# Kernel tuning notes

Hardware: AMD Instinct MI355X
Metric: run time of the kernel (lower is better)

Reference implementation:

```python
import jax, jax.numpy as jnp
import numpy as np

B, S, DMAX, NMEL, DM, K = 8, 100, 12, 80, 128, 9
T = S * DMAX  # 1200 max mel frames
EPS = 1e-5  # BatchNorm eps (eval mode, running_mean=0, running_var=1)


def setup_inputs() -> dict:
    key = jax.random.key(0)
    ks = jax.random.split(key, 16)
    durations = jax.random.randint(ks[0], (B, S), 4, DMAX + 1).astype(jnp.int32)
    mel_len = jnp.sum(durations, axis=1).astype(jnp.int32)
    src_len = jnp.full((B,), S, dtype=jnp.int32)
    mel = jax.random.normal(ks[1], (B, T, NMEL), dtype=jnp.float32)
    # conv stack params (xavier-ish uniform)
    s1 = float(np.sqrt(6.0 / (1 * K + DM * K)))
    w1 = jax.random.uniform(ks[2], (DM, 1, 1, K), minval=-s1, maxval=s1, dtype=jnp.float32)
    g1 = 1.0 + 0.1 * jax.random.normal(ks[3], (DM,), dtype=jnp.float32)
    be1 = 0.1 * jax.random.normal(ks[4], (DM,), dtype=jnp.float32)
    s2 = float(np.sqrt(6.0 / (DM * K + 1 * K)))
    w2 = jax.random.uniform(ks[5], (1, DM, 1, K), minval=-s2, maxval=s2, dtype=jnp.float32)
    g2 = 1.0 + 0.1 * jax.random.normal(ks[6], (1,), dtype=jnp.float32)
    be2 = 0.1 * jax.random.normal(ks[7], (1,), dtype=jnp.float32)
    # BiGRU params (pytorch layout: gates [r|z|n] stacked -> 3*H rows)
    sh = float(1.0 / np.sqrt(DM))
    u = lambda k, shape: jax.random.uniform(k, shape, minval=-sh, maxval=sh, dtype=jnp.float32)
    w_ih_f = u(ks[8], (3 * DM, NMEL)); w_hh_f = u(ks[9], (3 * DM, DM))
    b_ih_f = u(ks[10], (3 * DM,));    b_hh_f = u(ks[11], (3 * DM,))
    w_ih_b = u(ks[12], (3 * DM, NMEL)); w_hh_b = u(ks[13], (3 * DM, DM))
    b_ih_b = u(ks[14], (3 * DM,));    b_hh_b = u(ks[15], (3 * DM,))
    return {"mel": mel, "durations": durations, "mel_len": mel_len, "src_len": src_len,
            "w1": w1, "g1": g1, "be1": be1, "w2": w2, "g2": g2, "be2": be2,
            "w_ih_f": w_ih_f, "w_hh_f": w_hh_f, "b_ih_f": b_ih_f, "b_hh_f": b_hh_f,
            "w_ih_b": w_ih_b, "w_hh_b": w_hh_b, "b_ih_b": b_ih_b, "b_hh_b": b_hh_b}


def _bn_eval(x, g, b):
    # eval-mode BatchNorm2d with running_mean=0, running_var=1; x [B,C,T,M]
    scale = g / jnp.sqrt(1.0 + EPS)
    return x * scale[None, :, None, None] + b[None, :, None, None]


def _gru_scan(xs_seq, reset_seq, w_hh, b_hh):
    # xs_seq [T,B,3H] precomputed input projections; reset_seq [T,B] 1.0 -> reset h to 0
    H = w_hh.shape[1]
    Bn = xs_seq.shape[1]

    def step(h, inp):
        xg, rst = inp
        h = h * (1.0 - rst)[:, None]
        hg = h @ w_hh.T + b_hh
        xr, xz, xn = jnp.split(xg, 3, axis=-1)
        hr, hz, hn = jnp.split(hg, 3, axis=-1)
        r = jax.nn.sigmoid(xr + hr)
        z = jax.nn.sigmoid(xz + hz)
        n = jnp.tanh(xn + r * hn)
        h_new = (1.0 - z) * n + z * h
        return h_new, h_new

    h0 = jnp.zeros((Bn, H), xs_seq.dtype)
    _, hs = jax.lax.scan(step, h0, (xs_seq, reset_seq))
    return hs  # [T,B,H]


def reference(mel, durations, mel_len, src_len, w1, g1, be1, w2, g2, be2,
              w_ih_f, w_hh_f, b_ih_f, b_hh_f, w_ih_b, w_hh_b, b_ih_b, b_hh_b):
    pad = (K - 1) // 2
    # conv stack: kernel (1,K) mixes only the mel-channel axis -> apply to full mel once
    x = mel[:, None, :, :]  # [B,1,T,M]
    x = jax.lax.conv_general_dilated(x, w1, (1, 1), [(0, 0), (pad, pad)])
    x = jax.nn.relu(_bn_eval(x, g1, be1))
    x = jax.lax.conv_general_dilated(x, w2, (1, 1), [(0, 0), (pad, pad)])
    x = jax.nn.relu(_bn_eval(x, g2, be2))
    x = x[:, 0]  # [B,T,M]

    # segment boundaries from durations (all phones valid here, durations > 0)
    cum = jnp.cumsum(durations, axis=1)      # [B,S]
    starts = cum - durations                 # segment start frame per phone
    ends = cum - 1                           # segment end frame per phone
    bidx = jnp.arange(B)[:, None]
    start_mask = jnp.zeros((B, T), x.dtype).at[bidx, starts].set(1.0)
    end_mask = jnp.zeros((B, T), x.dtype).at[bidx, ends].set(1.0)

    # forward direction: reset h at segment starts, read h at segment ends
    xf = jnp.einsum('btm,gm->tbg', x, w_ih_f) + b_ih_f
    Hf = _gru_scan(xf, start_mask.T, w_hh_f, b_hh_f)           # [T,B,H]
    # backward direction: scan reversed time, reset at original segment ends
    xb = jnp.einsum('btm,gm->tbg', x, w_ih_b) + b_ih_b
    Hb = _gru_scan(xb[::-1], end_mask.T[::-1], w_hh_b, b_hh_b)[::-1]  # [T,B,H], orig time

    hf = jnp.take_along_axis(jnp.transpose(Hf, (1, 0, 2)), ends[..., None], axis=1)    # [B,S,H]
    hb = jnp.take_along_axis(jnp.transpose(Hb, (1, 0, 2)), starts[..., None], axis=1)  # [B,S,H]
    out = jnp.concatenate([hf, hb], axis=-1)  # [B,S,2H]
    valid = (jnp.arange(S)[None, :] < src_len[:, None])[..., None]
    return jnp.where(valid, out, 0.0)
```

## Files before the change

kernel.cpp:

```cpp
#include <hip/hip_runtime.h>
#include <math.h>

#define BB   8
#define SS   100
#define TT   1200
#define NM   80
#define DMC  128
#define KK   9
#define G3   384
#define NROW (BB*TT)

typedef __attribute__((ext_vector_type(8))) short short8;
typedef __attribute__((ext_vector_type(4))) float f32x4;

__device__ __forceinline__ float sigmoid_(float v) { return 1.f / (1.f + __expf(-v)); }
__device__ __forceinline__ float tanh_(float v) {
    float a = fabsf(v);
    float e = __expf(-2.f * a);
    float t = (1.f - e) / (1.f + e);
    return copysignf(t, v);
}
__device__ __forceinline__ unsigned short f2bf(float f) {
    unsigned int u = __float_as_uint(f);
    unsigned int r = (u + 0x7fffu + ((u >> 16) & 1u)) >> 16;
    return (unsigned short)r;
}

__global__ __launch_bounds__(1024) void k_prep(
    const float* __restrict__ whf, const float* __restrict__ whb,
    const float* __restrict__ wif, const float* __restrict__ wib,
    const float* __restrict__ bf, const float* __restrict__ bbv,
    const int* __restrict__ dur,
    unsigned short* __restrict__ wph, unsigned short* __restrict__ wpl,
    unsigned short* __restrict__ wih_h, unsigned short* __restrict__ wih_l,
    float* __restrict__ biasc, int* __restrict__ starts) {
    int blk = blockIdx.x;
    int tid = threadIdx.x;
    if (blk < 12) {
        int idx = blk * 1024 + tid;
        int lane = idx & 63;
        int k32  = (idx >> 6) & 3;
        int tau  = (idx >> 8) % 24;
        int dir  = idx / (24 * 4 * 64);
        const float* w = dir ? whb : whf;
        int g = tau * 16 + (lane & 15);
        int kbase = k32 * 32 + (lane >> 4) * 8;
#pragma unroll
        for (int j = 0; j < 8; j++) {
            float v = w[g * DMC + kbase + j];
            unsigned short hi = f2bf(v);
            float hif = __uint_as_float(((unsigned)hi) << 16);
            unsigned short lo = f2bf(v - hif);
            wph[idx * 8 + j] = hi;
            wpl[idx * 8 + j] = lo;
        }
    } else if (blk < 21) {
        int idx = (blk - 12) * 1024 + tid;
        int lane = idx & 63;
        int ks   = (idx >> 6) % 3;
        int tau  = idx / (3 * 64);
        int gate = tau * 16 + (lane & 15);
        int kb   = ks * 32 + (lane >> 4) * 8;
        const float* w = (gate < G3) ? (wif + gate * NM) : (wib + (gate - G3) * NM);
#pragma unroll
        for (int j = 0; j < 8; j++) {
            int k = kb + j;
            float v = (k < NM) ? w[k] : 0.f;
            unsigned short hi = f2bf(v);
            float hif = __uint_as_float(((unsigned)hi) << 16);
            unsigned short lo = f2bf(v - hif);
            wih_h[idx * 8 + j] = hi;
            wih_l[idx * 8 + j] = lo;
        }
    } else {
        __shared__ int buf[BB][128];
        int s = tid & 127, b = tid >> 7;
        int v = (s < SS) ? dur[b * SS + s] : 0;
        buf[b][s] = v;
        __syncthreads();
        for (int off = 1; off < 128; off <<= 1) {
            int t = (s >= off) ? buf[b][s - off] : 0;
            __syncthreads();
            buf[b][s] += t;
            __syncthreads();
        }
        if (s < SS) starts[b * SS + s] = buf[b][s] - v;
        if (tid < 768) biasc[tid] = (tid < G3) ? bf[tid] : bbv[tid - G3];
    }
}

__global__ __launch_bounds__(256) void k_conv(
    const float* __restrict__ mel, const int* __restrict__ mel_len,
    const float* __restrict__ w1, const float* __restrict__ g1, const float* __restrict__ be1,
    const float* __restrict__ w2, const float* __restrict__ g2, const float* __restrict__ be2,
    float* __restrict__ xout) {
    int b = blockIdx.y;
    int t = blockIdx.x;
    int ml = mel_len[b];
    if (t >= ml) return;

    __shared__ __align__(16) float mp[96];
    __shared__ __align__(16) float part[8][84];

    int tid = threadIdx.x;
    int mq = tid >> 6, g = tid & 63;
    int ms = 20 * mq;
    const float inv_sqrt = 0.9999950000374997f;

    if (tid < 96) {
        float v = 0.f;
        if (tid >= 8 && tid < 88) v = mel[(b * TT + t) * NM + tid - 8];
        mp[tid] = v;
    }
    __syncthreads();

    float c[20];
#pragma unroll
    for (int m = 0; m < 20; m++) c[m] = 0.f;

#pragma unroll 1
    for (int dd = 0; dd < 2; dd++) {
        int d = g + 64 * dd;
        float sc = g1[d] * inv_sqrt;
        float w1r[KK], w2r[KK];
#pragma unroll
        for (int k = 0; k < KK; k++) { w1r[k] = w1[d * KK + k] * sc; w2r[k] = w2[d * KK + k]; }
        float sb = be1[d];

        float mw[12];
        {
            const float4* p4 = (const float4*)(mp + ms);
            float4 a = p4[0], bq = p4[1], cq = p4[2];
            mw[0]=a.x;  mw[1]=a.y;  mw[2]=a.z;  mw[3]=a.w;
            mw[4]=bq.x; mw[5]=bq.y; mw[6]=bq.z; mw[7]=bq.w;
            mw[8]=cq.x; mw[9]=cq.y; mw[10]=cq.z; mw[11]=cq.w;
        }
#pragma unroll
        for (int ch = 0; ch < 7; ch++) {
#pragma unroll
            for (int jj = 0; jj < 4; jj++) {
                int off = ch * 4 + jj;
                float yv = sb;
#pragma unroll
                for (int k = 0; k < KK; k++) yv = fmaf(w1r[k], mw[jj + k], yv);
                yv = fmaxf(yv, 0.f);
                int j = ms + off;
                if (j < 4 || j >= 84) yv = 0.f;
#pragma unroll
                for (int k = 0; k < KK; k++) {
                    int mo = off - k;
                    if (mo >= 0 && mo < 20) c[mo] = fmaf(w2r[k], yv, c[mo]);
                }
            }
            if (ch < 6) {
#pragma unroll
                for (int q = 0; q < 8; q++) mw[q] = mw[q + 4];
                const float4* p4 = (const float4*)(mp + ms + ch * 4 + 12);
                float4 a = p4[0];
                mw[8]=a.x; mw[9]=a.y; mw[10]=a.z; mw[11]=a.w;
            }
        }
    }

#pragma unroll
    for (int m = 0; m < 20; m++) {
        c[m] += __shfl_xor(c[m], 1);
        c[m] += __shfl_xor(c[m], 2);
        c[m] += __shfl_xor(c[m], 4);
    }
    if ((g & 7) == 0) {
        int p = g >> 3;
#pragma unroll
        for (int m = 0; m < 20; m += 4)
            *(float4*)&part[p][ms + m] = make_float4(c[m], c[m+1], c[m+2], c[m+3]);
    }
    __syncthreads();

    if (tid < 80) {
        float s = 0.f;
#pragma unroll
        for (int p = 0; p < 8; p++) s += part[p][tid];
        float v = fmaxf(0.f, fmaf(s, g2[0] * inv_sqrt, be2[0]));
        xout[(b * TT + t) * NM + tid] = v;
    }
}

__global__ __launch_bounds__(256) void k_proj(
    const float* __restrict__ x,
    const unsigned short* __restrict__ wih_h, const unsigned short* __restrict__ wih_l,
    const float* __restrict__ biasc,
    float* __restrict__ xall) {
    __shared__ short8 bhs[2 * 3 * 64];
    __shared__ short8 bls[2 * 3 * 64];

    int tid = threadIdx.x;
    int wave = tid >> 6, lane = tid & 63, quad = lane >> 4;
    int row0 = blockIdx.x * 32;
    int tau0 = blockIdx.y * 24;

    for (int i = tid; i < 2 * 3 * 64; i += 256) {
        int rg = i / 192, rem = i - rg * 192;
        int ks = rem >> 6, ln = rem & 63;
        int row = row0 + rg * 16 + (ln & 15);
        int kb = ks * 32 + (ln >> 4) * 8;
        short8 hi8, lo8;
#pragma unroll
        for (int j = 0; j < 8; j++) {
            int k = kb + j;
            float v = (k < NM) ? x[row * NM + k] : 0.f;
            unsigned short hi = f2bf(v);
            float hif = __uint_as_float(((unsigned)hi) << 16);
            hi8[j] = (short)hi;
            lo8[j] = (short)f2bf(v - hif);
        }
        bhs[i] = hi8;
        bls[i] = lo8;
    }
    __syncthreads();

    const short8* wih_h8 = (const short8*)wih_h;
    const short8* wih_l8 = (const short8*)wih_l;

    for (int tt = 0; tt < 6; tt++) {
        int tau = tau0 + wave * 6 + tt;
        short8 Ah[3], Al[3];
#pragma unroll
        for (int ks = 0; ks < 3; ks++) {
            int ia = (tau * 3 + ks) * 64 + lane;
            Ah[ks] = wih_h8[ia];
            Al[ks] = wih_l8[ia];
        }
        f32x4 acc0 = (f32x4){0.f,0.f,0.f,0.f}, acc1 = (f32x4){0.f,0.f,0.f,0.f};
#pragma unroll
        for (int ks = 0; ks < 3; ks++) {
            short8 Bh0 = bhs[ks * 64 + lane],       Bl0 = bls[ks * 64 + lane];
            short8 Bh1 = bhs[192 + ks * 64 + lane], Bl1 = bls[192 + ks * 64 + lane];
            acc0 = __builtin_amdgcn_mfma_f32_16x16x32_bf16(Ah[ks], Bh0, acc0, 0, 0, 0);
            acc0 = __builtin_amdgcn_mfma_f32_16x16x32_bf16(Ah[ks], Bl0, acc0, 0, 0, 0);
            acc0 = __builtin_amdgcn_mfma_f32_16x16x32_bf16(Al[ks], Bh0, acc0, 0, 0, 0);
            acc1 = __builtin_amdgcn_mfma_f32_16x16x32_bf16(Ah[ks], Bh1, acc1, 0, 0, 0);
            acc1 = __builtin_amdgcn_mfma_f32_16x16x32_bf16(Ah[ks], Bl1, acc1, 0, 0, 0);
            acc1 = __builtin_amdgcn_mfma_f32_16x16x32_bf16(Al[ks], Bh1, acc1, 0, 0, 0);
        }
        float4 bias4 = *(const float4*)&biasc[tau * 16 + quad * 4];
        int ga = tau * 16 + quad * 4;
        int rowA = row0 + (lane & 15);
        float4 o0 = make_float4(acc0[0] + bias4.x, acc0[1] + bias4.y,
                                acc0[2] + bias4.z, acc0[3] + bias4.w);
        *(float4*)&xall[rowA * 768 + ga] = o0;
        int rowB = rowA + 16;
        float4 o1 = make_float4(acc1[0] + bias4.x, acc1[1] + bias4.y,
                                acc1[2] + bias4.z, acc1[3] + bias4.w);
        *(float4*)&xall[rowB * 768 + ga] = o1;
    }
}

__global__ __launch_bounds__(512) void k_gru(
    const float* __restrict__ xall,
    const unsigned short* __restrict__ wph, const unsigned short* __restrict__ wpl,
    const int* __restrict__ dur_all, const int* __restrict__ starts,
    const int* __restrict__ src_len,
    const float* __restrict__ bhf, const float* __restrict__ bhb,
    float* __restrict__ out) {
    int sblk = blockIdx.x;
    int b    = blockIdx.y;
    int dir  = blockIdx.z;
    int s0 = sblk * 16;

    __shared__ __align__(16) unsigned short hbh[2][2048];
    __shared__ __align__(16) unsigned short hbl[2][2048];

    int tid  = threadIdx.x;
    int wave = tid >> 6, lane = tid & 63;
    int quad = lane >> 4, seg = lane & 15;

    for (int i = tid; i < 2048; i += 512) {
        hbh[0][i] = 0; hbl[0][i] = 0; hbh[1][i] = 0; hbl[1][i] = 0;
    }

    short8 Ah[3][4], Al[3][4];
    const short8* wph8 = (const short8*)wph;
    const short8* wpl8 = (const short8*)wpl;
#pragma unroll
    for (int tt = 0; tt < 3; tt++)
#pragma unroll
        for (int k32 = 0; k32 < 4; k32++) {
            int tau = wave + 8 * tt;
            int idx = ((dir * 24 + tau) * 4 + k32) * 64 + lane;
            Ah[tt][k32] = wph8[idx];
            Al[tt][k32] = wpl8[idx];
        }

    int s = s0 + seg;
    int sd = (s < SS) ? dur_all[b * SS + s] : 0;
    int st = (s < SS) ? starts[b * SS + s]  : 0;
    int slb = src_len[b];
    const float* bh = dir ? bhb : bhf;
    int j0 = wave * 16 + quad * 4;
    float4 bhr = *(const float4*)&bh[j0];
    float4 bhz = *(const float4*)&bh[DMC + j0];
    float4 bhn = *(const float4*)&bh[2 * DMC + j0];
    float4 h = make_float4(0.f, 0.f, 0.f, 0.f);

    int idx8 = (j0 >> 5) * 64 + ((j0 >> 3) & 3) * 16 + seg;
    int wbase = idx8 * 8 + (j0 & 7);

    __syncthreads();

    for (int i = 0; i < 12; i++) {
        int p = i & 1;
        bool act = (i < sd);

        float4 xr = make_float4(0.f,0.f,0.f,0.f), xz = xr, xn = xr;
        if (act) {
            int t = dir ? (st + sd - 1 - i) : (st + i);
            const float* xrow = xall + (size_t)(b * TT + t) * 768 + dir * G3 + j0;
            xr = *(const float4*)&xrow[0];
            xz = *(const float4*)&xrow[DMC];
            xn = *(const float4*)&xrow[2 * DMC];
        }

        f32x4 acc[3];
#pragma unroll
        for (int tt = 0; tt < 3; tt++) acc[tt] = (f32x4){0.f, 0.f, 0.f, 0.f};
#pragma unroll
        for (int k32 = 0; k32 < 4; k32++) {
            short8 Bh = ((const short8*)hbh[p])[k32 * 64 + lane];
            short8 Bl = ((const short8*)hbl[p])[k32 * 64 + lane];
#pragma unroll
            for (int tt = 0; tt < 3; tt++) {
                acc[tt] = __builtin_amdgcn_mfma_f32_16x16x32_bf16(Ah[tt][k32], Bh, acc[tt], 0, 0, 0);
                acc[tt] = __builtin_amdgcn_mfma_f32_16x16x32_bf16(Ah[tt][k32], Bl, acc[tt], 0, 0, 0);
                acc[tt] = __builtin_amdgcn_mfma_f32_16x16x32_bf16(Al[tt][k32], Bh, acc[tt], 0, 0, 0);
            }
        }

        if (act) {
            float hv[4] = {h.x, h.y, h.z, h.w};
            float xrv[4] = {xr.x, xr.y, xr.z, xr.w};
            float xzv[4] = {xz.x, xz.y, xz.z, xz.w};
            float xnv[4] = {xn.x, xn.y, xn.z, xn.w};
            float bhrv[4] = {bhr.x, bhr.y, bhr.z, bhr.w};
            float bhzv[4] = {bhz.x, bhz.y, bhz.z, bhz.w};
            float bhnv[4] = {bhn.x, bhn.y, bhn.z, bhn.w};
#pragma unroll
            for (int cmp = 0; cmp < 4; cmp++) {
                float r = sigmoid_(xrv[cmp] + acc[0][cmp] + bhrv[cmp]);
                float z = sigmoid_(xzv[cmp] + acc[1][cmp] + bhzv[cmp]);
                float n = tanh_(xnv[cmp] + r * (acc[2][cmp] + bhnv[cmp]));
                hv[cmp] = (1.f - z) * n + z * hv[cmp];
            }
            h = make_float4(hv[0], hv[1], hv[2], hv[3]);
            if (i == sd - 1) {
                float4 vout = (s < slb) ? h : make_float4(0.f, 0.f, 0.f, 0.f);
                *(float4*)&out[(b * SS + s) * (2 * DMC) + dir * DMC + j0] = vout;
            }
        }

        {
            float hv[4] = {h.x, h.y, h.z, h.w};
            ushort4 hi4, lo4;
            unsigned short hs_[4], ls_[4];
#pragma unroll
            for (int cmp = 0; cmp < 4; cmp++) {
                unsigned short hi = f2bf(hv[cmp]);
                float hif = __uint_as_float(((unsigned)hi) << 16);
                hs_[cmp] = hi;
                ls_[cmp] = f2bf(hv[cmp] - hif);
            }
            hi4 = make_ushort4(hs_[0], hs_[1], hs_[2], hs_[3]);
            lo4 = make_ushort4(ls_[0], ls_[1], ls_[2], ls_[3]);
            *(ushort4*)&hbh[1 - p][wbase] = hi4;
            *(ushort4*)&hbl[1 - p][wbase] = lo4;
        }
        __syncthreads();
    }
}

extern "C" void kernel_launch(void* const* d_in, const int* in_sizes, int n_in,
                              void* d_out, int out_size, void* d_ws, size_t ws_size,
                              hipStream_t stream) {
    const float* mel      = (const float*)d_in[0];
    const int*   durations= (const int*)  d_in[1];
    const int*   mel_len  = (const int*)  d_in[2];
    const int*   src_len  = (const int*)  d_in[3];
    const float* w1       = (const float*)d_in[4];
    const float* g1       = (const float*)d_in[5];
    const float* be1      = (const float*)d_in[6];
    const float* w2       = (const float*)d_in[7];
    const float* g2       = (const float*)d_in[8];
    const float* be2      = (const float*)d_in[9];
    const float* w_ih_f   = (const float*)d_in[10];
    const float* w_hh_f   = (const float*)d_in[11];
    const float* b_ih_f   = (const float*)d_in[12];
    const float* b_hh_f   = (const float*)d_in[13];
    const float* w_ih_b   = (const float*)d_in[14];
    const float* w_hh_b   = (const float*)d_in[15];
    const float* b_ih_b   = (const float*)d_in[16];
    const float* b_hh_b   = (const float*)d_in[17];
    float* out = (float*)d_out;

    float* x    = (float*)d_ws;
    float* xall = x + NROW * NM;
    unsigned short* wph   = (unsigned short*)(xall + NROW * 768);
    unsigned short* wpl   = wph + 2 * 24 * 4 * 64 * 8;
    unsigned short* wih_h = wpl + 2 * 24 * 4 * 64 * 8;
    unsigned short* wih_l = wih_h + 48 * 3 * 64 * 8;
    float* biasc = (float*)(wih_l + 48 * 3 * 64 * 8);
    int*   starts= (int*)(biasc + 768);

    k_prep<<<22, 1024, 0, stream>>>(w_hh_f, w_hh_b, w_ih_f, w_ih_b, b_ih_f, b_ih_b,
                                    durations, wph, wpl, wih_h, wih_l, biasc, starts);
    k_conv<<<dim3(TT, BB), 256, 0, stream>>>(mel, mel_len, w1, g1, be1, w2, g2, be2, x);
    k_proj<<<dim3(NROW / 32, 2), 256, 0, stream>>>(x, wih_h, wih_l, biasc, xall);
    k_gru<<<dim3(7, 8, 2), 512, 0, stream>>>(xall, wph, wpl, durations, starts, src_len,
                                             b_hh_f, b_hh_b, out);
}
```

Before: 181.8 us.

## Rewrite conv stack on MFMA with split-bf16 weights and activations

The two-layer conv stack moves from scalar FMA loops to bf16 MFMA instructions. Each fp32 value is split into a hi and a lo bf16 part and three MFMAs are issued per tile to keep near-fp32 accuracy. k_prep gains two blocks that pre-pack the BN-scaled conv1 weights and the transposed conv2 weights into the MFMA operand layout. Intermediate activations are staged in shared memory, and conv2 is computed as per-tap partial sums that are then summed along diagonals. This adds shared-memory traffic and extra precision-split work per frame.

```diff
diff --git a/kernel.cpp b/kernel.cpp
--- a/kernel.cpp
+++ b/kernel.cpp
@@ -31,9 +31,13 @@
     const float* __restrict__ wif, const float* __restrict__ wib,
     const float* __restrict__ bf, const float* __restrict__ bbv,
     const int* __restrict__ dur,
+    const float* __restrict__ w1, const float* __restrict__ g1,
+    const float* __restrict__ w2,
     unsigned short* __restrict__ wph, unsigned short* __restrict__ wpl,
     unsigned short* __restrict__ wih_h, unsigned short* __restrict__ wih_l,
-    float* __restrict__ biasc, int* __restrict__ starts) {
+    float* __restrict__ biasc, int* __restrict__ starts,
+    unsigned short* __restrict__ w1fh, unsigned short* __restrict__ w1fl,
+    unsigned short* __restrict__ w2th, unsigned short* __restrict__ w2tl) {
     int blk = blockIdx.x;
     int tid = threadIdx.x;
     if (blk < 12) {
@@ -72,7 +76,7 @@
             wih_h[idx * 8 + j] = hi;
             wih_l[idx * 8 + j] = lo;
         }
-    } else {
+    } else if (blk == 21) {
         __shared__ int buf[BB][128];
         int s = tid & 127, b = tid >> 7;
         int v = (s < SS) ? dur[b * SS + s] : 0;
@@ -86,102 +90,149 @@
         }
         if (s < SS) starts[b * SS + s] = buf[b][s] - v;
         if (tid < 768) biasc[tid] = (tid < G3) ? bf[tid] : bbv[tid - G3];
+    } else if (blk == 22) {
+        if (tid < 512) {
+            int dt = tid >> 6, lane = tid & 63;
+            int d = dt * 16 + (lane & 15);
+            float sc = g1[d] * 0.9999950000374997f;
+#pragma unroll
+            for (int j = 0; j < 8; j++) {
+                int k = (lane >> 4) * 8 + j;
+                float v = (k < KK) ? w1[d * KK + k] * sc : 0.f;
+                unsigned short hi = f2bf(v);
+                float hif = __uint_as_float(((unsigned)hi) << 16);
+                w1fh[tid * 8 + j] = hi;
+                w1fl[tid * 8 + j] = f2bf(v - hif);
+            }
+        }
+    } else {
+        if (tid < 256) {
+            int k32 = tid >> 6, lane = tid & 63;
+            int kp = lane & 15;
+#pragma unroll
+            for (int j = 0; j < 8; j++) {
+                int d = k32 * 32 + (lane >> 4) * 8 + j;
+                float v = (kp < KK) ? w2[d * KK + kp] : 0.f;
+                unsigned short hi = f2bf(v);
+                float hif = __uint_as_float(((unsigned)hi) << 16);
+                w2th[tid * 8 + j] = hi;
+                w2tl[tid * 8 + j] = f2bf(v - hif);
+            }
+        }
     }
 }
 
 __global__ __launch_bounds__(256) void k_conv(
     const float* __restrict__ mel, const int* __restrict__ mel_len,
-    const float* __restrict__ w1, const float* __restrict__ g1, const float* __restrict__ be1,
-    const float* __restrict__ w2, const float* __restrict__ g2, const float* __restrict__ be2,
+    const unsigned short* __restrict__ w1fh, const unsigned short* __restrict__ w1fl,
+    const float* __restrict__ be1,
+    const unsigned short* __restrict__ w2th, const unsigned short* __restrict__ w2tl,
+    const float* __restrict__ g2, const float* __restrict__ be2,
     float* __restrict__ xout) {
-    int b = blockIdx.y;
-    int t = blockIdx.x;
-    int ml = mel_len[b];
-    if (t >= ml) return;
-
-    __shared__ __align__(16) float mp[96];
-    __shared__ __align__(16) float part[8][84];
-
-    int tid = threadIdx.x;
-    int mq = tid >> 6, g = tid & 63;
-    int ms = 20 * mq;
-    const float inv_sqrt = 0.9999950000374997f;
+    int b = blockIdx.y, t = blockIdx.x;
+    if (t >= mel_len[b]) return;
+
+    __shared__ __align__(16) unsigned short mh[96], mlo[96];
+    __shared__ __align__(16) unsigned short y1h[96][136], y1l[96][136];
+    __shared__ __align__(16) float gl[96][13];
+
+    int tid = threadIdx.x, wave = tid >> 6, lane = tid & 63;
+    int quad = lane >> 4, col = lane & 15;
+    const float invs = 0.9999950000374997f;
 
     if (tid < 96) {
-        float v = 0.f;
-        if (tid >= 8 && tid < 88) v = mel[(b * TT + t) * NM + tid - 8];
-        mp[tid] = v;
+        float v = (tid >= 4 && tid < 84) ? mel[(b * TT + t) * NM + tid - 4] : 0.f;
+        unsigned short hi = f2bf(v);
+        mh[tid]  = hi;
+        mlo[tid] = f2bf(v - __uint_as_float(((unsigned)hi) << 16));
+    }
+    for (int i = tid; i < 16 * 136; i += 256) {
+        int r = i / 136, c2 = i - r * 136;
+        int row = (r < 4) ? r : 80 + r;
+        y1h[row][c2] = 0; y1l[row][c2] = 0;
     }
     __syncthreads();
 
-    float c[20];
-#pragma unroll
-    for (int m = 0; m < 20; m++) c[m] = 0.f;
-
-#pragma unroll 1
+    const short8* w1fh8 = (const short8*)w1fh;
+    const short8* w1fl8 = (const short8*)w1fl;
+    short8 a1h[2], a1l[2];
+    float4 bb[2];
+#pragma unroll
     for (int dd = 0; dd < 2; dd++) {
-        int d = g + 64 * dd;
-        float sc = g1[d] * inv_sqrt;
-        float w1r[KK], w2r[KK];
-#pragma unroll
-        for (int k = 0; k < KK; k++) { w1r[k] = w1[d * KK + k] * sc; w2r[k] = w2[d * KK + k]; }
-        float sb = be1[d];
-
-        float mw[12];
-        {
-            const float4* p4 = (const float4*)(mp + ms);
-            float4 a = p4[0], bq = p4[1], cq = p4[2];
-            mw[0]=a.x;  mw[1]=a.y;  mw[2]=a.z;  mw[3]=a.w;
-            mw[4]=bq.x; mw[5]=bq.y; mw[6]=bq.z; mw[7]=bq.w;
-            mw[8]=cq.x; mw[9]=cq.y; mw[10]=cq.z; mw[11]=cq.w;
-        }
-#pragma unroll
-        for (int ch = 0; ch < 7; ch++) {
-#pragma unroll
-            for (int jj = 0; jj < 4; jj++) {
-                int off = ch * 4 + jj;
-                float yv = sb;
-#pragma unroll
-                for (int k = 0; k < KK; k++) yv = fmaf(w1r[k], mw[jj + k], yv);
-                yv = fmaxf(yv, 0.f);
-                int j = ms + off;
-                if (j < 4 || j >= 84) yv = 0.f;
-#pragma unroll
-                for (int k = 0; k < KK; k++) {
-                    int mo = off - k;
-                    if (mo >= 0 && mo < 20) c[mo] = fmaf(w2r[k], yv, c[mo]);
-                }
-            }
-            if (ch < 6) {
-#pragma unroll
-                for (int q = 0; q < 8; q++) mw[q] = mw[q + 4];
-                const float4* p4 = (const float4*)(mp + ms + ch * 4 + 12);
-                float4 a = p4[0];
-                mw[8]=a.x; mw[9]=a.y; mw[10]=a.z; mw[11]=a.w;
-            }
-        }
-    }
-
-#pragma unroll
-    for (int m = 0; m < 20; m++) {
-        c[m] += __shfl_xor(c[m], 1);
-        c[m] += __shfl_xor(c[m], 2);
-        c[m] += __shfl_xor(c[m], 4);
-    }
-    if ((g & 7) == 0) {
-        int p = g >> 3;
-#pragma unroll
-        for (int m = 0; m < 20; m += 4)
-            *(float4*)&part[p][ms + m] = make_float4(c[m], c[m+1], c[m+2], c[m+3]);
+        int dt = 2 * wave + dd;
+        a1h[dd] = w1fh8[dt * 64 + lane];
+        a1l[dd] = w1fl8[dt * 64 + lane];
+        bb[dd]  = *(const float4*)&be1[dt * 16 + quad * 4];
+    }
+#pragma unroll
+    for (int nt = 0; nt < 5; nt++) {
+        int mbase = nt * 16 + col;
+        short8 Bh = {0,0,0,0,0,0,0,0}, Bl = {0,0,0,0,0,0,0,0};
+        if (quad == 0) {
+#pragma unroll
+            for (int j = 0; j < 8; j++) {
+                Bh[j] = (short)mh[mbase + j];
+                Bl[j] = (short)mlo[mbase + j];
+            }
+        } else if (quad == 1) {
+            Bh[0] = (short)mh[mbase + 8];
+            Bl[0] = (short)mlo[mbase + 8];
+        }
+#pragma unroll
+        for (int dd = 0; dd < 2; dd++) {
+            f32x4 acc = (f32x4){0.f, 0.f, 0.f, 0.f};
+            acc = __builtin_amdgcn_mfma_f32_16x16x32_bf16(a1h[dd], Bh, acc, 0, 0, 0);
+            acc = __builtin_amdgcn_mfma_f32_16x16x32_bf16(a1h[dd], Bl, acc, 0, 0, 0);
+            acc = __builtin_amdgcn_mfma_f32_16x16x32_bf16(a1l[dd], Bh, acc, 0, 0, 0);
+            int i = mbase + 4;
+            int dbase = (2 * wave + dd) * 16 + quad * 4;
+            float bbv[4] = {bb[dd].x, bb[dd].y, bb[dd].z, bb[dd].w};
+            unsigned short hs4[4], ls4[4];
+#pragma unroll
+            for (int reg = 0; reg < 4; reg++) {
+                float y = fmaxf(acc[reg] + bbv[reg], 0.f);
+                unsigned short hi = f2bf(y);
+                hs4[reg] = hi;
+                ls4[reg] = f2bf(y - __uint_as_float(((unsigned)hi) << 16));
+            }
+            *(ushort4*)&y1h[i][dbase] = make_ushort4(hs4[0], hs4[1], hs4[2], hs4[3]);
+            *(ushort4*)&y1l[i][dbase] = make_ushort4(ls4[0], ls4[1], ls4[2], ls4[3]);
+        }
     }
     __syncthreads();
 
-    if (tid < 80) {
+    const short8* w2th8 = (const short8*)w2th;
+    const short8* w2tl8 = (const short8*)w2tl;
+    short8 a2h[4], a2l[4];
+#pragma unroll
+    for (int k32 = 0; k32 < 4; k32++) {
+        a2h[k32] = w2th8[k32 * 64 + lane];
+        a2l[k32] = w2tl8[k32 * 64 + lane];
+    }
+    for (int nn = wave; nn < 6; nn += 4) {
+        int i = nn * 16 + col;
+        f32x4 acc = (f32x4){0.f, 0.f, 0.f, 0.f};
+#pragma unroll
+        for (int k32 = 0; k32 < 4; k32++) {
+            short8 Bh = *(const short8*)&y1h[i][k32 * 32 + quad * 8];
+            short8 Bl = *(const short8*)&y1l[i][k32 * 32 + quad * 8];
+            acc = __builtin_amdgcn_mfma_f32_16x16x32_bf16(a2h[k32], Bh, acc, 0, 0, 0);
+            acc = __builtin_amdgcn_mfma_f32_16x16x32_bf16(a2h[k32], Bl, acc, 0, 0, 0);
+            acc = __builtin_amdgcn_mfma_f32_16x16x32_bf16(a2l[k32], Bh, acc, 0, 0, 0);
+        }
+#pragma unroll
+        for (int reg = 0; reg < 4; reg++) {
+            int kp = quad * 4 + reg;
+            if (kp < KK) gl[i][kp] = acc[reg];
+        }
+    }
+    __syncthreads();
+
+    if (tid < NM) {
         float s = 0.f;
 #pragma unroll
-        for (int p = 0; p < 8; p++) s += part[p][tid];
-        float v = fmaxf(0.f, fmaf(s, g2[0] * inv_sqrt, be2[0]));
-        xout[(b * TT + t) * NM + tid] = v;
+        for (int k = 0; k < KK; k++) s += gl[tid + k][k];
+        xout[(b * TT + t) * NM + tid] = fmaxf(0.f, fmaf(s, g2[0] * invs, be2[0]));
     }
 }
 
@@ -359,7 +410,6 @@
 
         {
             float hv[4] = {h.x, h.y, h.z, h.w};
-            ushort4 hi4, lo4;
             unsigned short hs_[4], ls_[4];
 #pragma unroll
             for (int cmp = 0; cmp < 4; cmp++) {
@@ -368,10 +418,8 @@
                 hs_[cmp] = hi;
                 ls_[cmp] = f2bf(hv[cmp] - hif);
             }
-            hi4 = make_ushort4(hs_[0], hs_[1], hs_[2], hs_[3]);
-            lo4 = make_ushort4(ls_[0], ls_[1], ls_[2], ls_[3]);
-            *(ushort4*)&hbh[1 - p][wbase] = hi4;
-            *(ushort4*)&hbl[1 - p][wbase] = lo4;
+            *(ushort4*)&hbh[1 - p][wbase] = make_ushort4(hs_[0], hs_[1], hs_[2], hs_[3]);
+            *(ushort4*)&hbl[1 - p][wbase] = make_ushort4(ls_[0], ls_[1], ls_[2], ls_[3]);
         }
         __syncthreads();
     }
@@ -408,10 +456,17 @@
     unsigned short* wih_l = wih_h + 48 * 3 * 64 * 8;
     float* biasc = (float*)(wih_l + 48 * 3 * 64 * 8);
     int*   starts= (int*)(biasc + 768);
-
-    k_prep<<<22, 1024, 0, stream>>>(w_hh_f, w_hh_b, w_ih_f, w_ih_b, b_ih_f, b_ih_b,
-                                    durations, wph, wpl, wih_h, wih_l, biasc, starts);
-    k_conv<<<dim3(TT, BB), 256, 0, stream>>>(mel, mel_len, w1, g1, be1, w2, g2, be2, x);
+    unsigned short* w1fh = (unsigned short*)(starts + 800);
+    unsigned short* w1fl = w1fh + 512 * 8;
+    unsigned short* w2th = w1fl + 512 * 8;
+    unsigned short* w2tl = w2th + 256 * 8;
+
+    k_prep<<<24, 1024, 0, stream>>>(w_hh_f, w_hh_b, w_ih_f, w_ih_b, b_ih_f, b_ih_b,
+                                    durations, w1, g1, w2,
+                                    wph, wpl, wih_h, wih_l, biasc, starts,
+                                    w1fh, w1fl, w2th, w2tl);
+    k_conv<<<dim3(TT, BB), 256, 0, stream>>>(mel, mel_len, w1fh, w1fl, be1,
+                                             w2th, w2tl, g2, be2, x);
     k_proj<<<dim3(NROW / 32, 2), 256, 0, stream>>>(x, wih_h, wih_l, biasc, xall);
     k_gru<<<dim3(7, 8, 2), 512, 0, stream>>>(xall, wph, wpl, durations, starts, src_len,
                                              b_hh_f, b_hh_b, out);
```

Result: slower. 192.4 us (+5.8%).

## Fuse GRU input projection into recurrent kernel, dropping xall intermediate

Applied to the files above, without the earlier changes.

Removes the separate k_proj kernel and the large xall buffer in global memory. Each GRU step now computes the input projection in-kernel with MFMA, using W_ih fragments held in registers and mel-frame data double-buffered in shared memory, prefetched one step ahead. This saves a kernel launch and the write and read-back of the intermediate, but adds MFMA work and register pressure to the serial recurrence. The b_ih and b_hh biases for r and z are pre-summed.

```diff
diff --git a/kernel.cpp b/kernel.cpp
--- a/kernel.cpp
+++ b/kernel.cpp
@@ -185,79 +185,11 @@
     }
 }
 
-__global__ __launch_bounds__(256) void k_proj(
+__global__ __launch_bounds__(512, 2) void k_gru(
     const float* __restrict__ x,
+    const unsigned short* __restrict__ wph, const unsigned short* __restrict__ wpl,
     const unsigned short* __restrict__ wih_h, const unsigned short* __restrict__ wih_l,
     const float* __restrict__ biasc,
-    float* __restrict__ xall) {
-    __shared__ short8 bhs[2 * 3 * 64];
-    __shared__ short8 bls[2 * 3 * 64];
-
-    int tid = threadIdx.x;
-    int wave = tid >> 6, lane = tid & 63, quad = lane >> 4;
-    int row0 = blockIdx.x * 32;
-    int tau0 = blockIdx.y * 24;
-
-    for (int i = tid; i < 2 * 3 * 64; i += 256) {
-        int rg = i / 192, rem = i - rg * 192;
-        int ks = rem >> 6, ln = rem & 63;
-        int row = row0 + rg * 16 + (ln & 15);
-        int kb = ks * 32 + (ln >> 4) * 8;
-        short8 hi8, lo8;
-#pragma unroll
-        for (int j = 0; j < 8; j++) {
-            int k = kb + j;
-            float v = (k < NM) ? x[row * NM + k] : 0.f;
-            unsigned short hi = f2bf(v);
-            float hif = __uint_as_float(((unsigned)hi) << 16);
-            hi8[j] = (short)hi;
-            lo8[j] = (short)f2bf(v - hif);
-        }
-        bhs[i] = hi8;
-        bls[i] = lo8;
-    }
-    __syncthreads();
-
-    const short8* wih_h8 = (const short8*)wih_h;
-    const short8* wih_l8 = (const short8*)wih_l;
-
-    for (int tt = 0; tt < 6; tt++) {
-        int tau = tau0 + wave * 6 + tt;
-        short8 Ah[3], Al[3];
-#pragma unroll
-        for (int ks = 0; ks < 3; ks++) {
-            int ia = (tau * 3 + ks) * 64 + lane;
-            Ah[ks] = wih_h8[ia];
-            Al[ks] = wih_l8[ia];
-        }
-        f32x4 acc0 = (f32x4){0.f,0.f,0.f,0.f}, acc1 = (f32x4){0.f,0.f,0.f,0.f};
-#pragma unroll
-        for (int ks = 0; ks < 3; ks++) {
-            short8 Bh0 = bhs[ks * 64 + lane],       Bl0 = bls[ks * 64 + lane];
-            short8 Bh1 = bhs[192 + ks * 64 + lane], Bl1 = bls[192 + ks * 64 + lane];
-            acc0 = __builtin_amdgcn_mfma_f32_16x16x32_bf16(Ah[ks], Bh0, acc0, 0, 0, 0);
-            acc0 = __builtin_amdgcn_mfma_f32_16x16x32_bf16(Ah[ks], Bl0, acc0, 0, 0, 0);
-            acc0 = __builtin_amdgcn_mfma_f32_16x16x32_bf16(Al[ks], Bh0, acc0, 0, 0, 0);
-            acc1 = __builtin_amdgcn_mfma_f32_16x16x32_bf16(Ah[ks], Bh1, acc1, 0, 0, 0);
-            acc1 = __builtin_amdgcn_mfma_f32_16x16x32_bf16(Ah[ks], Bl1, acc1, 0, 0, 0);
-            acc1 = __builtin_amdgcn_mfma_f32_16x16x32_bf16(Al[ks], Bh1, acc1, 0, 0, 0);
-        }
-        float4 bias4 = *(const float4*)&biasc[tau * 16 + quad * 4];
-        int ga = tau * 16 + quad * 4;
-        int rowA = row0 + (lane & 15);
-        float4 o0 = make_float4(acc0[0] + bias4.x, acc0[1] + bias4.y,
-                                acc0[2] + bias4.z, acc0[3] + bias4.w);
-        *(float4*)&xall[rowA * 768 + ga] = o0;
-        int rowB = rowA + 16;
-        float4 o1 = make_float4(acc1[0] + bias4.x, acc1[1] + bias4.y,
-                                acc1[2] + bias4.z, acc1[3] + bias4.w);
-        *(float4*)&xall[rowB * 768 + ga] = o1;
-    }
-}
-
-__global__ __launch_bounds__(512) void k_gru(
-    const float* __restrict__ xall,
-    const unsigned short* __restrict__ wph, const unsigned short* __restrict__ wpl,
     const int* __restrict__ dur_all, const int* __restrict__ starts,
     const int* __restrict__ src_len,
     const float* __restrict__ bhf, const float* __restrict__ bhb,
@@ -269,14 +201,20 @@
 
     __shared__ __align__(16) unsigned short hbh[2][2048];
     __shared__ __align__(16) unsigned short hbl[2][2048];
+    __shared__ __align__(16) short8 xbh[2][192];
+    __shared__ __align__(16) short8 xbl[2][192];
+    __shared__ int sdur[16], sstart[16];
 
     int tid  = threadIdx.x;
     int wave = tid >> 6, lane = tid & 63;
     int quad = lane >> 4, seg = lane & 15;
 
-    for (int i = tid; i < 2048; i += 512) {
-        hbh[0][i] = 0; hbl[0][i] = 0; hbh[1][i] = 0; hbl[1][i] = 0;
-    }
+    if (tid < 16) {
+        int ss = s0 + tid;
+        sdur[tid]   = (ss < SS) ? dur_all[b * SS + ss] : 0;
+        sstart[tid] = (ss < SS) ? starts[b * SS + ss]  : 0;
+    }
+    for (int i = tid; i < 2048; i += 512) { hbh[0][i] = 0; hbl[0][i] = 0; }
 
     short8 Ah[3][4], Al[3][4];
     const short8* wph8 = (const short8*)wph;
@@ -285,69 +223,113 @@
     for (int tt = 0; tt < 3; tt++)
 #pragma unroll
         for (int k32 = 0; k32 < 4; k32++) {
-            int tau = wave + 8 * tt;
-            int idx = ((dir * 24 + tau) * 4 + k32) * 64 + lane;
+            int idx = ((dir * 24 + wave + 8 * tt) * 4 + k32) * 64 + lane;
             Ah[tt][k32] = wph8[idx];
             Al[tt][k32] = wpl8[idx];
+        }
+    short8 Gh[3][3], Gl[3][3];
+    const short8* wih_h8 = (const short8*)wih_h;
+    const short8* wih_l8 = (const short8*)wih_l;
+#pragma unroll
+    for (int tt = 0; tt < 3; tt++)
+#pragma unroll
+        for (int ks = 0; ks < 3; ks++) {
+            int idx = ((dir * 24 + wave + 8 * tt) * 3 + ks) * 64 + lane;
+            Gh[tt][ks] = wih_h8[idx];
+            Gl[tt][ks] = wih_l8[idx];
         }
 
     int s = s0 + seg;
     int sd = (s < SS) ? dur_all[b * SS + s] : 0;
     int st = (s < SS) ? starts[b * SS + s]  : 0;
     int slb = src_len[b];
-    const float* bh = dir ? bhb : bhf;
+    const float* bih = biasc + dir * G3;
+    const float* bhh = dir ? bhb : bhf;
     int j0 = wave * 16 + quad * 4;
-    float4 bhr = *(const float4*)&bh[j0];
-    float4 bhz = *(const float4*)&bh[DMC + j0];
-    float4 bhn = *(const float4*)&bh[2 * DMC + j0];
+    float4 i_r = *(const float4*)&bih[j0];
+    float4 i_z = *(const float4*)&bih[DMC + j0];
+    float4 bxn = *(const float4*)&bih[2 * DMC + j0];
+    float4 h_r = *(const float4*)&bhh[j0];
+    float4 h_z = *(const float4*)&bhh[DMC + j0];
+    float4 bhn = *(const float4*)&bhh[2 * DMC + j0];
+    float4 br = make_float4(i_r.x + h_r.x, i_r.y + h_r.y, i_r.z + h_r.z, i_r.w + h_r.w);
+    float4 bz = make_float4(i_z.x + h_z.x, i_z.y + h_z.y, i_z.z + h_z.z, i_z.w + h_z.w);
     float4 h = make_float4(0.f, 0.f, 0.f, 0.f);
 
     int idx8 = (j0 >> 5) * 64 + ((j0 >> 3) & 3) * 16 + seg;
     int wbase = idx8 * 8 + (j0 & 7);
 
+    __syncthreads();
+
+    if (tid < 192) {
+        int ks = tid >> 6, ln = tid & 63;
+        int sg = ln & 15, qq = ln >> 4;
+        int kb = ks * 32 + qq * 8;
+        short8 hi8 = {0,0,0,0,0,0,0,0}, lo8 = {0,0,0,0,0,0,0,0};
+        if (kb < NM && 0 < sdur[sg]) {
+            int t = dir ? (sstart[sg] + sdur[sg] - 1) : sstart[sg];
+            const float* xr = x + (size_t)(b * TT + t) * NM + kb;
+#pragma unroll
+            for (int j = 0; j < 8; j++) {
+                float v = xr[j];
+                unsigned short hi = f2bf(v);
+                hi8[j] = (short)hi;
+                lo8[j] = (short)f2bf(v - __uint_as_float(((unsigned)hi) << 16));
+            }
+        }
+        xbh[0][tid] = hi8;
+        xbl[0][tid] = lo8;
+    }
     __syncthreads();
 
     for (int i = 0; i < 12; i++) {
         int p = i & 1;
         bool act = (i < sd);
 
-        float4 xr = make_float4(0.f,0.f,0.f,0.f), xz = xr, xn = xr;
-        if (act) {
-            int t = dir ? (st + sd - 1 - i) : (st + i);
-            const float* xrow = xall + (size_t)(b * TT + t) * 768 + dir * G3 + j0;
-            xr = *(const float4*)&xrow[0];
-            xz = *(const float4*)&xrow[DMC];
-            xn = *(const float4*)&xrow[2 * DMC];
-        }
-
-        f32x4 acc[3];
-#pragma unroll
-        for (int tt = 0; tt < 3; tt++) acc[tt] = (f32x4){0.f, 0.f, 0.f, 0.f};
+        f32x4 acc0 = (f32x4){0.f,0.f,0.f,0.f};
+        f32x4 acc1 = (f32x4){0.f,0.f,0.f,0.f};
+        f32x4 acc2 = (f32x4){0.f,0.f,0.f,0.f};
+        f32x4 acc3 = (f32x4){0.f,0.f,0.f,0.f};
+#pragma unroll
+        for (int ks = 0; ks < 3; ks++) {
+            short8 Bxh = xbh[p][ks * 64 + lane];
+            short8 Bxl = xbl[p][ks * 64 + lane];
+            acc0 = __builtin_amdgcn_mfma_f32_16x16x32_bf16(Gh[0][ks], Bxh, acc0, 0, 0, 0);
+            acc0 = __builtin_amdgcn_mfma_f32_16x16x32_bf16(Gh[0][ks], Bxl, acc0, 0, 0, 0);
+            acc0 = __builtin_amdgcn_mfma_f32_16x16x32_bf16(Gl[0][ks], Bxh, acc0, 0, 0, 0);
+            acc1 = __builtin_amdgcn_mfma_f32_16x16x32_bf16(Gh[1][ks], Bxh, acc1, 0, 0, 0);
+            acc1 = __builtin_amdgcn_mfma_f32_16x16x32_bf16(Gh[1][ks], Bxl, acc1, 0, 0, 0);
+            acc1 = __builtin_amdgcn_mfma_f32_16x16x32_bf16(Gl[1][ks], Bxh, acc1, 0, 0, 0);
+            acc3 = __builtin_amdgcn_mfma_f32_16x16x32_bf16(Gh[2][ks], Bxh, acc3, 0, 0, 0);
+            acc3 = __builtin_amdgcn_mfma_f32_16x16x32_bf16(Gh[2][ks], Bxl, acc3, 0, 0, 0);
+            acc3 = __builtin_amdgcn_mfma_f32_16x16x32_bf16(Gl[2][ks], Bxh, acc3, 0, 0, 0);
+        }
 #pragma unroll
         for (int k32 = 0; k32 < 4; k32++) {
             short8 Bh = ((const short8*)hbh[p])[k32 * 64 + lane];
             short8 Bl = ((const short8*)hbl[p])[k32 * 64 + lane];
-#pragma unroll
-            for (int tt = 0; tt < 3; tt++) {
-                acc[tt] = __builtin_amdgcn_mfma_f32_16x16x32_bf16(Ah[tt][k32], Bh, acc[tt], 0, 0, 0);
-                acc[tt] = __builtin_amdgcn_mfma_f32_16x16x32_bf16(Ah[tt][k32], Bl, acc[tt], 0, 0, 0);
-                acc[tt] = __builtin_amdgcn_mfma_f32_16x16x32_bf16(Al[tt][k32], Bh, acc[tt], 0, 0, 0);
-            }
+            acc0 = __builtin_amdgcn_mfma_f32_16x16x32_bf16(Ah[0][k32], Bh, acc0, 0, 0, 0);
+            acc0 = __builtin_amdgcn_mfma_f32_16x16x32_bf16(Ah[0][k32], Bl, acc0, 0, 0, 0);
+            acc0 = __builtin_amdgcn_mfma_f32_16x16x32_bf16(Al[0][k32], Bh, acc0, 0, 0, 0);
+            acc1 = __builtin_amdgcn_mfma_f32_16x16x32_bf16(Ah[1][k32], Bh, acc1, 0, 0, 0);
+            acc1 = __builtin_amdgcn_mfma_f32_16x16x32_bf16(Ah[1][k32], Bl, acc1, 0, 0, 0);
+            acc1 = __builtin_amdgcn_mfma_f32_16x16x32_bf16(Al[1][k32], Bh, acc1, 0, 0, 0);
+            acc2 = __builtin_amdgcn_mfma_f32_16x16x32_bf16(Ah[2][k32], Bh, acc2, 0, 0, 0);
+            acc2 = __builtin_amdgcn_mfma_f32_16x16x32_bf16(Ah[2][k32], Bl, acc2, 0, 0, 0);
+            acc2 = __builtin_amdgcn_mfma_f32_16x16x32_bf16(Al[2][k32], Bh, acc2, 0, 0, 0);
         }
 
         if (act) {
-            float hv[4] = {h.x, h.y, h.z, h.w};
-            float xrv[4] = {xr.x, xr.y, xr.z, xr.w};
-            float xzv[4] = {xz.x, xz.y, xz.z, xz.w};
-            float xnv[4] = {xn.x, xn.y, xn.z, xn.w};
-            float bhrv[4] = {bhr.x, bhr.y, bhr.z, bhr.w};
-            float bhzv[4] = {bhz.x, bhz.y, bhz.z, bhz.w};
-            float bhnv[4] = {bhn.x, bhn.y, bhn.z, bhn.w};
+            float hv[4]  = {h.x, h.y, h.z, h.w};
+            float brv[4] = {br.x, br.y, br.z, br.w};
+            float bzv[4] = {bz.x, bz.y, bz.z, bz.w};
+            float bxv[4] = {bxn.x, bxn.y, bxn.z, bxn.w};
+            float bhv[4] = {bhn.x, bhn.y, bhn.z, bhn.w};
 #pragma unroll
             for (int cmp = 0; cmp < 4; cmp++) {
-                float r = sigmoid_(xrv[cmp] + acc[0][cmp] + bhrv[cmp]);
-                float z = sigmoid_(xzv[cmp] + acc[1][cmp] + bhzv[cmp]);
-                float n = tanh_(xnv[cmp] + r * (acc[2][cmp] + bhnv[cmp]));
+                float r = sigmoid_(acc0[cmp] + brv[cmp]);
+                float z = sigmoid_(acc1[cmp] + bzv[cmp]);
+                float n = tanh_(acc3[cmp] + bxv[cmp] + r * (acc2[cmp] + bhv[cmp]));
                 hv[cmp] = (1.f - z) * n + z * hv[cmp];
             }
             h = make_float4(hv[0], hv[1], hv[2], hv[3]);
@@ -359,7 +341,6 @@
 
         {
             float hv[4] = {h.x, h.y, h.z, h.w};
-            ushort4 hi4, lo4;
             unsigned short hs_[4], ls_[4];
 #pragma unroll
             for (int cmp = 0; cmp < 4; cmp++) {
@@ -368,10 +349,30 @@
                 hs_[cmp] = hi;
                 ls_[cmp] = f2bf(hv[cmp] - hif);
             }
-            hi4 = make_ushort4(hs_[0], hs_[1], hs_[2], hs_[3]);
-            lo4 = make_ushort4(ls_[0], ls_[1], ls_[2], ls_[3]);
-            *(ushort4*)&hbh[1 - p][wbase] = hi4;
-            *(ushort4*)&hbl[1 - p][wbase] = lo4;
+            *(ushort4*)&hbh[1 - p][wbase] = make_ushort4(hs_[0], hs_[1], hs_[2], hs_[3]);
+            *(ushort4*)&hbl[1 - p][wbase] = make_ushort4(ls_[0], ls_[1], ls_[2], ls_[3]);
+        }
+
+        if (tid < 192) {
+            int i2 = i + 1;
+            int ks = tid >> 6, ln = tid & 63;
+            int sg = ln & 15, qq = ln >> 4;
+            int kb = ks * 32 + qq * 8;
+            short8 hi8 = {0,0,0,0,0,0,0,0}, lo8 = {0,0,0,0,0,0,0,0};
+            int d2 = sdur[sg];
+            if (kb < NM && i2 < d2) {
+                int t = dir ? (sstart[sg] + d2 - 1 - i2) : (sstart[sg] + i2);
+                const float* xr = x + (size_t)(b * TT + t) * NM + kb;
+#pragma unroll
+                for (int j = 0; j < 8; j++) {
+                    float v = xr[j];
+                    unsigned short hi = f2bf(v);
+                    hi8[j] = (short)hi;
+                    lo8[j] = (short)f2bf(v - __uint_as_float(((unsigned)hi) << 16));
+                }
+            }
+            xbh[1 - p][tid] = hi8;
+            xbl[1 - p][tid] = lo8;
         }
         __syncthreads();
     }
@@ -401,8 +402,7 @@
     float* out = (float*)d_out;
 
     float* x    = (float*)d_ws;
-    float* xall = x + NROW * NM;
-    unsigned short* wph   = (unsigned short*)(xall + NROW * 768);
+    unsigned short* wph   = (unsigned short*)(x + NROW * NM);
     unsigned short* wpl   = wph + 2 * 24 * 4 * 64 * 8;
     unsigned short* wih_h = wpl + 2 * 24 * 4 * 64 * 8;
     unsigned short* wih_l = wih_h + 48 * 3 * 64 * 8;
@@ -412,7 +412,7 @@
     k_prep<<<22, 1024, 0, stream>>>(w_hh_f, w_hh_b, w_ih_f, w_ih_b, b_ih_f, b_ih_b,
                                     durations, wph, wpl, wih_h, wih_l, biasc, starts);
     k_conv<<<dim3(TT, BB), 256, 0, stream>>>(mel, mel_len, w1, g1, be1, w2, g2, be2, x);
-    k_proj<<<dim3(NROW / 32, 2), 256, 0, stream>>>(x, wih_h, wih_l, biasc, xall);
-    k_gru<<<dim3(7, 8, 2), 512, 0, stream>>>(xall, wph, wpl, durations, starts, src_len,
+    k_gru<<<dim3(7, 8, 2), 512, 0, stream>>>(x, wph, wpl, wih_h, wih_l, biasc,
+                                             durations, starts, src_len,
                                              b_hh_f, b_hh_b, out);
 }
```

Measured after the change: 166.9 us. 1.09x faster.
